# Kernel optimization log

Hardware: AMD Instinct MI355X
Metric: run time of the kernel (lower is better)

Reference implementation:

```python
import jax, jax.numpy as jnp
import numpy as np

L, M, K, H, F, D = 8, 32768, 8, 128, 32, 3  # fronts, nodes/front, in-degree, hidden, feat, depth-branches


def _resnet(x, w1, b1, w2, b2, w3, b3):
    # resnet module: lay3(tanh(lay2(tanh(lay1(x)))) + x)
    h1 = jnp.tanh(x @ w1 + b1)
    h2 = jnp.tanh(h1 @ w2 + b2)
    return (h2 + x) @ w3 + b3


def setup_inputs() -> dict:
    key = jax.random.key(0)
    ks = iter(jax.random.split(key, 80))

    def nrm(shape, fan_in):
        return jax.random.normal(next(ks), shape, jnp.float32) / np.float32(np.sqrt(fan_in))

    def bias(shape):
        return 0.01 * jax.random.normal(next(ks), shape, jnp.float32)

    inp = {}
    inp["node_feats"] = jax.random.normal(next(ks), (L, M, F), jnp.float32)
    inp["pred_idx"] = jax.random.randint(next(ks), (L - 1, M, K), 0, M, jnp.int32)
    inp["embed_w"] = nrm((F, H), F); inp["embed_b"] = bias((H,))
    # d{1,2,3}_mp_bwd and d{1,2,3}_mp_bwd1 : per-depth pair of H-resnets, stacked [D,2,...]
    inp["mp_w1"] = nrm((D, 2, H, H), H); inp["mp_b1"] = bias((D, 2, H))
    inp["mp_w2"] = nrm((D, 2, H, H), H); inp["mp_b2"] = bias((D, 2, H))
    inp["mp_w3"] = nrm((D, 2, H, H), H); inp["mp_b3"] = bias((D, 2, H))
    for p in ("comb", "node"):  # d*_comb_embed(+1), d*_node_embeds(+1)
        inp[p + "_wide_w1"] = nrm((D, 2 * H, 2 * H), 2 * H); inp[p + "_wide_b1"] = bias((D, 2 * H))
        inp[p + "_wide_w2"] = nrm((D, 2 * H, 2 * H), 2 * H); inp[p + "_wide_b2"] = bias((D, 2 * H))
        inp[p + "_wide_w3"] = nrm((D, 2 * H, H), 2 * H);     inp[p + "_wide_b3"] = bias((D, H))
        inp[p + "_h_w1"] = nrm((D, H, H), H); inp[p + "_h_b1"] = bias((D, H))
        inp[p + "_h_w2"] = nrm((D, H, H), H); inp[p + "_h_b2"] = bias((D, H))
        inp[p + "_h_w3"] = nrm((D, H, H), H); inp[p + "_h_b3"] = bias((D, H))
    return inp


def reference(node_feats, pred_idx, embed_w, embed_b,
              mp_w1, mp_b1, mp_w2, mp_b2, mp_w3, mp_b3,
              comb_wide_w1, comb_wide_b1, comb_wide_w2, comb_wide_b2, comb_wide_w3, comb_wide_b3,
              comb_h_w1, comb_h_b1, comb_h_w2, comb_h_b2, comb_h_w3, comb_h_b3,
              node_wide_w1, node_wide_b1, node_wide_w2, node_wide_b2, node_wide_w3, node_wide_b3,
              node_h_w1, node_h_b1, node_h_w2, node_h_b2, node_h_w3, node_h_b3):
    # front 0 (topological roots): apply_func only -> tanh(embed_op(feats))
    e = jnp.tanh(node_feats[0] @ embed_w + embed_b)          # [M, H]
    outs = [e]
    prev = e
    for l in range(1, L):
        d = min(l - 1, 2)                                    # bwd_depth branch (d1/d2/d3)
        # msg_func + redux_func: gather mailbox from predecessor front, sum-reduce, MLP
        s = prev[pred_idx[l - 1]].sum(axis=1)                # [M, K, H] -> [M, H]
        r = jnp.tanh(_resnet(s, mp_w1[d, 0], mp_b1[d, 0], mp_w2[d, 0], mp_b2[d, 0], mp_w3[d, 0], mp_b3[d, 0]))
        r = jnp.tanh(_resnet(r, mp_w1[d, 1], mp_b1[d, 1], mp_w2[d, 1], mp_b2[d, 1], mp_w3[d, 1], mp_b3[d, 1]))
        # apply_func: embed, comb branch (bwd_node_embeds is all-zero for not-yet-processed nodes),
        # then node_embeds branch on cat(embeds, msgs_redux)
        e = jnp.tanh(node_feats[l] @ embed_w + embed_b)
        c = jnp.concatenate([e, jnp.zeros_like(e)], axis=-1)  # [M, 2H]
        e = jnp.tanh(_resnet(c, comb_wide_w1[d], comb_wide_b1[d], comb_wide_w2[d], comb_wide_b2[d], comb_wide_w3[d], comb_wide_b3[d]))
        e = jnp.tanh(_resnet(e, comb_h_w1[d], comb_h_b1[d], comb_h_w2[d], comb_h_b2[d], comb_h_w3[d], comb_h_b3[d]))
        c2 = jnp.concatenate([e, r], axis=-1)                 # [M, 2H]
        e = jnp.tanh(_resnet(c2, node_wide_w1[d], node_wide_b1[d], node_wide_w2[d], node_wide_b2[d], node_wide_w3[d], node_wide_b3[d]))
        e = jnp.tanh(_resnet(e, node_h_w1[d], node_h_b1[d], node_h_w2[d], node_h_b2[d], node_h_w3[d], node_h_b3[d]))
        outs.append(e)
        prev = e
    return jnp.stack(outs)                                    # graph.ndata['bwd_node_embeds'] : [L, M, H]
```

## Files before the change

kernel.cpp:

```cpp
#include <hip/hip_runtime.h>
#include <hip/hip_bf16.h>

#define M_NODES 32768

using f16x8 = __attribute__((ext_vector_type(8))) _Float16;
using f32x4 = __attribute__((ext_vector_type(4))) float;
typedef unsigned short u16;
typedef unsigned int   u32;

__device__ __forceinline__ u16 f2h(float f){
  _Float16 h = (_Float16)f;
  return __builtin_bit_cast(u16, h);
}
__device__ __forceinline__ float h2f(u16 h){
  return (float)__builtin_bit_cast(_Float16, h);
}
__device__ __forceinline__ float tanh_fast(float x){
  float t = __builtin_amdgcn_exp2f(x * 2.8853900817779268f);
  return 1.0f - 2.0f * __builtin_amdgcn_rcpf(t + 1.0f);
}

struct PrepPtrs { const float* p[16]; };

__global__ void prep_kernel(PrepPtrs pp, u16* ws){
  const int Bc[16] = {1,6,6,6,3,3,3,3,3,3,3,3,3,3,3,3};
  const int Kc[16] = {32,128,128,128,256,256,256,128,128,128,256,256,256,128,128,128};
  const int Nc[16] = {128,128,128,128,256,256,128,128,128,128,256,256,128,128,128,128};
  const int tot = 1576960;
  for (int i = blockIdx.x*blockDim.x + threadIdx.x; i < tot; i += gridDim.x*blockDim.x){
    int e = i, s = 0;
    while (true){ int sz = Bc[s]*Kc[s]*Nc[s]; if (e < sz) break; e -= sz; ++s; }
    int K = Kc[s], N = Nc[s];
    int kn = K*N;
    int b = e / kn; int r2 = e - b*kn;
    int n = r2 / K; int k = r2 - n*K;
    float v = pp.p[s][(size_t)b*kn + (size_t)k*N + n];
    ws[i] = f2h(v);
  }
}

__global__ __launch_bounds__(256) void front0_kernel(const float* __restrict__ feats,
                                                     const float* __restrict__ ew,
                                                     const float* __restrict__ eb,
                                                     float* __restrict__ out){
  __shared__ float fl[2048];
  const int brow = blockIdx.x * 64;
  const float* f0 = feats + (size_t)brow*32;
#pragma unroll
  for (int it = 0; it < 2; ++it){
    int idx = threadIdx.x + it*256;
    *(float4*)(&fl[idx*4]) = *(const float4*)(f0 + idx*4);
  }
  __syncthreads();
  const int col = threadIdx.x & 127, rh = threadIdx.x >> 7;
  float w[32];
#pragma unroll
  for (int k = 0; k < 32; ++k) w[k] = ew[k*128 + col];
  const float bv = eb[col];
  for (int r = 0; r < 32; ++r){
    int row = rh*32 + r;
    float acc = bv;
#pragma unroll
    for (int k = 0; k < 32; ++k) acc += fl[row*32 + k] * w[k];
    out[(size_t)(brow + row)*128 + col] = tanh_fast(acc);
  }
}

template<int KLOOP, int N, int WS, int AMODE, int RESMODE, int OUTMODE>
__device__ __forceinline__ void mm_stage(const u16* inA, u16* outB, const u16* resB,
                                         const u16* __restrict__ wt,
                                         const float* __restrict__ bias,
                                         float* gout, u16* WP)
{
  const int tid  = threadIdx.x;
  const int lane = tid & 63, wid = tid >> 6;
  const int mh = wid >> 2, nq = wid & 3;
  const int q = lane >> 4, c = lane & 15;
  constexpr int NT = N / 64;
  constexpr int NP = KLOOP / 32;
  const float* inAf = (const float*)inA;
  float*       outF = (float*)outB;
  const float* resF = (const float*)resB;

  f32x4 acc[4][NT];
#pragma unroll
  for (int m = 0; m < 4; ++m)
#pragma unroll
    for (int j = 0; j < NT; ++j) acc[m][j] = (f32x4){0.f,0.f,0.f,0.f};

  for (int kp = 0; kp < NP; ++kp){
#pragma unroll
    for (int it = 0; it < N/128; ++it){
      int tt = tid + it*512;
      int n = tt >> 2, ko = (tt & 3) * 8;
      uint4 v = *(const uint4*)(wt + (size_t)n*WS + kp*32 + ko);
      *(uint4*)(&WP[n*40 + ko]) = v;
    }
    __syncthreads();
    f16x8 bf[NT];
#pragma unroll
    for (int j = 0; j < NT; ++j){
      int nt = nq*2 + (j & 1) + (j >> 1) * 8;
      bf[j] = *(const f16x8*)(&WP[(nt*16 + c)*40 + q*8]);
    }
#pragma unroll
    for (int m = 0; m < 4; ++m){
      if (AMODE == 0){
        f16x8 af = *(const f16x8*)(&inA[(mh*64 + m*16 + c)*264 + kp*32 + q*8]);
#pragma unroll
        for (int j = 0; j < NT; ++j)
          acc[m][j] = __builtin_amdgcn_mfma_f32_16x16x32_f16(af, bf[j], acc[m][j], 0, 0, 0);
      } else {
        const float* ap = inAf + (mh*64 + m*16 + c)*132 + kp*32 + q*8;
        float4 x0 = *(const float4*)(ap);
        float4 x1 = *(const float4*)(ap + 4);
        float xs[8] = {x0.x,x0.y,x0.z,x0.w,x1.x,x1.y,x1.z,x1.w};
        f16x8 ah, al;
#pragma unroll
        for (int k = 0; k < 8; ++k){
          _Float16 hi = (_Float16)xs[k];
          ah[k] = hi;
          al[k] = (_Float16)(xs[k] - (float)hi);
        }
#pragma unroll
        for (int j = 0; j < NT; ++j){
          acc[m][j] = __builtin_amdgcn_mfma_f32_16x16x32_f16(ah, bf[j], acc[m][j], 0, 0, 0);
          acc[m][j] = __builtin_amdgcn_mfma_f32_16x16x32_f16(al, bf[j], acc[m][j], 0, 0, 0);
        }
      }
    }
    __syncthreads();
  }
#pragma unroll
  for (int j = 0; j < NT; ++j){
    int nt = nq*2 + (j & 1) + (j >> 1) * 8;
    int col = nt*16 + c;
    float bv = bias[col];
#pragma unroll
    for (int m = 0; m < 4; ++m){
#pragma unroll
      for (int r = 0; r < 4; ++r){
        int row = mh*64 + m*16 + q*4 + r;
        float v = tanh_fast(acc[m][j][r] + bv);
        if (RESMODE == 2)      v += h2f(resB[row*264 + col]);
        else if (RESMODE == 1){ if (col < 128) v += h2f(resB[row*264 + col]); }
        else if (RESMODE == 3) v += resF[row*132 + col];
        if (OUTMODE == 2)      gout[(size_t)row*128 + col] = v;
        else if (OUTMODE == 1) outF[row*132 + col] = v;
        else                   outB[row*264 + col] = f2h(v);
      }
    }
  }
}

__device__ __forceinline__ void embed_stage(const float* __restrict__ featsRow,
                                            u16* outB, const u16* __restrict__ wt,
                                            const float* __restrict__ bias, u16* WP)
{
  const int tid  = threadIdx.x;
  const int lane = tid & 63, wid = tid >> 6;
  const int mh = wid >> 2, nq = wid & 3;
  const int q = lane >> 4, c = lane & 15;
  {
    int n = tid >> 2, ko = (tid & 3) * 8;
    *(uint4*)(&WP[n*40 + ko]) = *(const uint4*)(wt + n*32 + ko);
  }
  __syncthreads();
  f16x8 bf[2];
#pragma unroll
  for (int j = 0; j < 2; ++j){
    int nt = nq*2 + j;
    bf[j] = *(const f16x8*)(&WP[(nt*16 + c)*40 + q*8]);
  }
  f32x4 acc[4][2];
#pragma unroll
  for (int m = 0; m < 4; ++m){ acc[m][0] = (f32x4){0,0,0,0}; acc[m][1] = (f32x4){0,0,0,0}; }
#pragma unroll
  for (int m = 0; m < 4; ++m){
    int row = mh*64 + m*16 + c;
    const float* fp = featsRow + (size_t)row*32 + q*8;
    float4 a0 = *(const float4*)(fp);
    float4 a1 = *(const float4*)(fp + 4);
    float xs[8] = {a0.x,a0.y,a0.z,a0.w,a1.x,a1.y,a1.z,a1.w};
    f16x8 ah, al;
#pragma unroll
    for (int k = 0; k < 8; ++k){
      _Float16 hi = (_Float16)xs[k];
      ah[k] = hi;
      al[k] = (_Float16)(xs[k] - (float)hi);
    }
#pragma unroll
    for (int j = 0; j < 2; ++j){
      acc[m][j] = __builtin_amdgcn_mfma_f32_16x16x32_f16(ah, bf[j], acc[m][j], 0, 0, 0);
      acc[m][j] = __builtin_amdgcn_mfma_f32_16x16x32_f16(al, bf[j], acc[m][j], 0, 0, 0);
    }
  }
  __syncthreads();
#pragma unroll
  for (int j = 0; j < 2; ++j){
    int nt = nq*2 + j;
    int col = nt*16 + c;
    float bv = bias[col];
#pragma unroll
    for (int m = 0; m < 4; ++m){
#pragma unroll
      for (int r = 0; r < 4; ++r){
        int row = mh*64 + m*16 + q*4 + r;
        outB[row*264 + col] = f2h(tanh_fast(acc[m][j][r] + bv));
      }
    }
  }
}

struct FrontArgs {
  const float* feats; const int* pred;
  const u16* ws;
  float* out;
  const float* embed_b;
  const float* mp_b1; const float* mp_b2; const float* mp_b3;
  const float* cw_b1; const float* cw_b2; const float* cw_b3;
  const float* ch_b1; const float* ch_b2; const float* ch_b3;
  const float* nw_b1; const float* nw_b2; const float* nw_b3;
  const float* nh_b1; const float* nh_b2; const float* nh_b3;
  int l, d;
};

__global__ __launch_bounds__(512, 1) void front_kernel(FrontArgs A)
{
  extern __shared__ u16 lds[];
  u16* P  = lds;
  u16* Q  = lds + 33792;
  u16* WP = lds + 67584;
  const int brow = blockIdx.x * 128;
  const int d = A.d;
  const u16* ws = A.ws;

  {
    float* Pf = (float*)P;
    const float* prev = A.out + (size_t)(A.l - 1) * M_NODES * 128;
    const int c4 = threadIdx.x & 31;
    const int r0 = threadIdx.x >> 5;
#pragma unroll
    for (int rr = 0; rr < 8; ++rr){
      int row = r0 + rr*16;
      const int* ip = A.pred + ((size_t)(A.l - 1) * M_NODES + brow + row) * 8;
      float sx=0.f, sy=0.f, sz=0.f, sw=0.f;
#pragma unroll
      for (int p = 0; p < 8; ++p){
        const float4 v = *(const float4*)(prev + (size_t)ip[p]*128 + c4*4);
        sx += v.x; sy += v.y; sz += v.z; sw += v.w;
      }
      float4 o = {sx, sy, sz, sw};
      *(float4*)(&Pf[row*132 + c4*4]) = o;
    }
  }
  __syncthreads();

  const int d0 = d*2, d1 = d*2 + 1;
  mm_stage<128,128,128, 1,0,0>(P, Q, nullptr, ws + 4096   + (size_t)d0*16384, A.mp_b1 + d0*128, nullptr, WP);
  mm_stage<128,128,128, 0,3,1>(Q, P, P,       ws + 102400 + (size_t)d0*16384, A.mp_b2 + d0*128, nullptr, WP);
  mm_stage<128,128,128, 1,0,0>(P, Q, nullptr, ws + 200704 + (size_t)d0*16384, A.mp_b3 + d0*128, nullptr, WP);
  mm_stage<128,128,128, 0,0,0>(Q, P, nullptr, ws + 4096   + (size_t)d1*16384, A.mp_b1 + d1*128, nullptr, WP);
  mm_stage<128,128,128, 0,2,1>(P, P, Q,       ws + 102400 + (size_t)d1*16384, A.mp_b2 + d1*128, nullptr, WP);
  mm_stage<128,128,128, 1,0,0>(P, Q + 128, nullptr, ws + 200704 + (size_t)d1*16384, A.mp_b3 + d1*128, nullptr, WP);

  embed_stage(A.feats + ((size_t)A.l * M_NODES + brow) * 32, Q, ws, A.embed_b, WP);

  mm_stage<128,256,256, 0,0,0>(Q, P, nullptr, ws + 299008 + (size_t)d*65536, A.cw_b1 + d*256, nullptr, WP);
  mm_stage<256,256,256, 0,1,0>(P, P, Q,       ws + 495616 + (size_t)d*65536, A.cw_b2 + d*256, nullptr, WP);
  mm_stage<256,128,256, 0,0,0>(P, Q, nullptr, ws + 692224 + (size_t)d*32768, A.cw_b3 + d*128, nullptr, WP);
  mm_stage<128,128,128, 0,0,0>(Q, P, nullptr, ws + 790528 + (size_t)d*16384, A.ch_b1 + d*128, nullptr, WP);
  mm_stage<128,128,128, 0,2,0>(P, P, Q,       ws + 839680 + (size_t)d*16384, A.ch_b2 + d*128, nullptr, WP);
  mm_stage<128,128,128, 0,0,0>(P, Q, nullptr, ws + 888832 + (size_t)d*16384, A.ch_b3 + d*128, nullptr, WP);
  mm_stage<256,256,256, 0,0,0>(Q, P, nullptr, ws + 937984  + (size_t)d*65536, A.nw_b1 + d*256, nullptr, WP);
  mm_stage<256,256,256, 0,2,0>(P, P, Q,       ws + 1134592 + (size_t)d*65536, A.nw_b2 + d*256, nullptr, WP);
  mm_stage<256,128,256, 0,0,0>(P, Q, nullptr, ws + 1331200 + (size_t)d*32768, A.nw_b3 + d*128, nullptr, WP);
  mm_stage<128,128,128, 0,0,0>(Q, P, nullptr, ws + 1429504 + (size_t)d*16384, A.nh_b1 + d*128, nullptr, WP);
  mm_stage<128,128,128, 0,2,0>(P, P, Q,       ws + 1478656 + (size_t)d*16384, A.nh_b2 + d*128, nullptr, WP);
  float* gout = A.out + ((size_t)A.l * M_NODES + brow) * 128;
  mm_stage<128,128,128, 0,0,2>(P, nullptr, nullptr, ws + 1527808 + (size_t)d*16384, A.nh_b3 + d*128, gout, WP);
}

extern "C" void kernel_launch(void* const* d_in, const int* in_sizes, int n_in,
                              void* d_out, int out_size, void* d_ws, size_t ws_size,
                              hipStream_t stream)
{
  (void)in_sizes; (void)n_in; (void)out_size; (void)ws_size;
  const float* feats = (const float*)d_in[0];
  const int*   pred  = (const int*)d_in[1];
  u16*   ws  = (u16*)d_ws;
  float* out = (float*)d_out;

  PrepPtrs pp;
  const int wIdx[16] = {2,4,6,8,10,12,14,16,18,20,22,24,26,28,30,32};
  for (int i = 0; i < 16; ++i) pp.p[i] = (const float*)d_in[wIdx[i]];
  prep_kernel<<<2048, 256, 0, stream>>>(pp, ws);

  front0_kernel<<<M_NODES/64, 256, 0, stream>>>(feats, (const float*)d_in[2], (const float*)d_in[3], out);

  const size_t LDSB = (size_t)(2*128*264 + 256*40) * sizeof(u16);
  (void)hipFuncSetAttribute((const void*)front_kernel,
                            hipFuncAttributeMaxDynamicSharedMemorySize, (int)LDSB);

  FrontArgs A;
  A.feats = feats; A.pred = pred; A.ws = ws; A.out = out;
  A.embed_b = (const float*)d_in[3];
  A.mp_b1 = (const float*)d_in[5];  A.mp_b2 = (const float*)d_in[7];  A.mp_b3 = (const float*)d_in[9];
  A.cw_b1 = (const float*)d_in[11]; A.cw_b2 = (const float*)d_in[13]; A.cw_b3 = (const float*)d_in[15];
  A.ch_b1 = (const float*)d_in[17]; A.ch_b2 = (const float*)d_in[19]; A.ch_b3 = (const float*)d_in[21];
  A.nw_b1 = (const float*)d_in[23]; A.nw_b2 = (const float*)d_in[25]; A.nw_b3 = (const float*)d_in[27];
  A.nh_b1 = (const float*)d_in[29]; A.nh_b2 = (const float*)d_in[31]; A.nh_b3 = (const float*)d_in[33];

  for (int l = 1; l < 8; ++l){
    A.l = l;
    A.d = (l - 1 < 2) ? (l - 1) : 2;
    front_kernel<<<M_NODES/128, 512, LDSB, stream>>>(A);
  }
}
```

Before: 772.0 us.

## Load weights directly into registers with prefetch; shrink blocks to 64 rows

Weight tiles are no longer staged through LDS. Each wave now loads its B fragments straight from global memory into registers, double-buffered two k-steps ahead, which removes the per-k-step __syncthreads pairs. Blocks shrink to 64 rows and 256 threads with a smaller LDS footprint, aiming for two blocks per CU. Barriers now sit only after each stage's epilogue and before in-place writes. The cost is more global/L2 traffic for weights, since they are no longer shared across the two row-halves, plus higher register pressure.

```diff
diff --git a/kernel.cpp b/kernel.cpp
--- a/kernel.cpp
+++ b/kernel.cpp
@@ -66,15 +66,14 @@
   }
 }
 
-template<int KLOOP, int N, int WS, int AMODE, int RESMODE, int OUTMODE>
+template<int KLOOP, int N, int WS, int AMODE, int RESMODE, int OUTMODE, bool INPLACE>
 __device__ __forceinline__ void mm_stage(const u16* inA, u16* outB, const u16* resB,
                                          const u16* __restrict__ wt,
                                          const float* __restrict__ bias,
-                                         float* gout, u16* WP)
+                                         float* gout)
 {
   const int tid  = threadIdx.x;
-  const int lane = tid & 63, wid = tid >> 6;
-  const int mh = wid >> 2, nq = wid & 3;
+  const int lane = tid & 63, nq = tid >> 6;
   const int q = lane >> 4, c = lane & 15;
   constexpr int NT = N / 64;
   constexpr int NP = KLOOP / 32;
@@ -82,36 +81,42 @@
   float*       outF = (float*)outB;
   const float* resF = (const float*)resB;
 
+  const u16* wrow[NT];
+#pragma unroll
+  for (int j = 0; j < NT; ++j){
+    int nt = nq*2 + (j & 1) + (j >> 1) * 8;
+    wrow[j] = wt + (size_t)(nt*16 + c)*WS + q*8;
+  }
+  f16x8 breg[2][NT];
+#pragma unroll
+  for (int j = 0; j < NT; ++j) breg[0][j] = *(const f16x8*)(wrow[j]);
+#pragma unroll
+  for (int j = 0; j < NT; ++j) breg[1][j] = *(const f16x8*)(wrow[j] + 32);
+
   f32x4 acc[4][NT];
 #pragma unroll
   for (int m = 0; m < 4; ++m)
 #pragma unroll
     for (int j = 0; j < NT; ++j) acc[m][j] = (f32x4){0.f,0.f,0.f,0.f};
 
+#pragma unroll
   for (int kp = 0; kp < NP; ++kp){
-#pragma unroll
-    for (int it = 0; it < N/128; ++it){
-      int tt = tid + it*512;
-      int n = tt >> 2, ko = (tt & 3) * 8;
-      uint4 v = *(const uint4*)(wt + (size_t)n*WS + kp*32 + ko);
-      *(uint4*)(&WP[n*40 + ko]) = v;
-    }
-    __syncthreads();
-    f16x8 bf[NT];
-#pragma unroll
-    for (int j = 0; j < NT; ++j){
-      int nt = nq*2 + (j & 1) + (j >> 1) * 8;
-      bf[j] = *(const f16x8*)(&WP[(nt*16 + c)*40 + q*8]);
+    f16x8 bc[NT];
+#pragma unroll
+    for (int j = 0; j < NT; ++j) bc[j] = breg[kp & 1][j];
+    if (kp + 2 < NP){
+#pragma unroll
+      for (int j = 0; j < NT; ++j) breg[kp & 1][j] = *(const f16x8*)(wrow[j] + (kp + 2)*32);
     }
 #pragma unroll
     for (int m = 0; m < 4; ++m){
       if (AMODE == 0){
-        f16x8 af = *(const f16x8*)(&inA[(mh*64 + m*16 + c)*264 + kp*32 + q*8]);
+        f16x8 af = *(const f16x8*)(&inA[(m*16 + c)*264 + kp*32 + q*8]);
 #pragma unroll
         for (int j = 0; j < NT; ++j)
-          acc[m][j] = __builtin_amdgcn_mfma_f32_16x16x32_f16(af, bf[j], acc[m][j], 0, 0, 0);
+          acc[m][j] = __builtin_amdgcn_mfma_f32_16x16x32_f16(af, bc[j], acc[m][j], 0, 0, 0);
       } else {
-        const float* ap = inAf + (mh*64 + m*16 + c)*132 + kp*32 + q*8;
+        const float* ap = inAf + (m*16 + c)*132 + kp*32 + q*8;
         float4 x0 = *(const float4*)(ap);
         float4 x1 = *(const float4*)(ap + 4);
         float xs[8] = {x0.x,x0.y,x0.z,x0.w,x1.x,x1.y,x1.z,x1.w};
@@ -124,13 +129,13 @@
         }
 #pragma unroll
         for (int j = 0; j < NT; ++j){
-          acc[m][j] = __builtin_amdgcn_mfma_f32_16x16x32_f16(ah, bf[j], acc[m][j], 0, 0, 0);
-          acc[m][j] = __builtin_amdgcn_mfma_f32_16x16x32_f16(al, bf[j], acc[m][j], 0, 0, 0);
+          acc[m][j] = __builtin_amdgcn_mfma_f32_16x16x32_f16(ah, bc[j], acc[m][j], 0, 0, 0);
+          acc[m][j] = __builtin_amdgcn_mfma_f32_16x16x32_f16(al, bc[j], acc[m][j], 0, 0, 0);
         }
       }
     }
-    __syncthreads();
-  }
+  }
+  if (INPLACE) __syncthreads();
 #pragma unroll
   for (int j = 0; j < NT; ++j){
     int nt = nq*2 + (j & 1) + (j >> 1) * 8;
@@ -140,7 +145,7 @@
     for (int m = 0; m < 4; ++m){
 #pragma unroll
       for (int r = 0; r < 4; ++r){
-        int row = mh*64 + m*16 + q*4 + r;
+        int row = m*16 + q*4 + r;
         float v = tanh_fast(acc[m][j][r] + bv);
         if (RESMODE == 2)      v += h2f(resB[row*264 + col]);
         else if (RESMODE == 1){ if (col < 128) v += h2f(resB[row*264 + col]); }
@@ -151,33 +156,28 @@
       }
     }
   }
+  __syncthreads();
 }
 
 __device__ __forceinline__ void embed_stage(const float* __restrict__ featsRow,
                                             u16* outB, const u16* __restrict__ wt,
-                                            const float* __restrict__ bias, u16* WP)
+                                            const float* __restrict__ bias)
 {
   const int tid  = threadIdx.x;
-  const int lane = tid & 63, wid = tid >> 6;
-  const int mh = wid >> 2, nq = wid & 3;
+  const int lane = tid & 63, nq = tid >> 6;
   const int q = lane >> 4, c = lane & 15;
-  {
-    int n = tid >> 2, ko = (tid & 3) * 8;
-    *(uint4*)(&WP[n*40 + ko]) = *(const uint4*)(wt + n*32 + ko);
-  }
-  __syncthreads();
   f16x8 bf[2];
 #pragma unroll
   for (int j = 0; j < 2; ++j){
     int nt = nq*2 + j;
-    bf[j] = *(const f16x8*)(&WP[(nt*16 + c)*40 + q*8]);
+    bf[j] = *(const f16x8*)(wt + (nt*16 + c)*32 + q*8);
   }
   f32x4 acc[4][2];
 #pragma unroll
   for (int m = 0; m < 4; ++m){ acc[m][0] = (f32x4){0,0,0,0}; acc[m][1] = (f32x4){0,0,0,0}; }
 #pragma unroll
   for (int m = 0; m < 4; ++m){
-    int row = mh*64 + m*16 + c;
+    int row = m*16 + c;
     const float* fp = featsRow + (size_t)row*32 + q*8;
     float4 a0 = *(const float4*)(fp);
     float4 a1 = *(const float4*)(fp + 4);
@@ -195,7 +195,6 @@
       acc[m][j] = __builtin_amdgcn_mfma_f32_16x16x32_f16(al, bf[j], acc[m][j], 0, 0, 0);
     }
   }
-  __syncthreads();
 #pragma unroll
   for (int j = 0; j < 2; ++j){
     int nt = nq*2 + j;
@@ -205,11 +204,12 @@
     for (int m = 0; m < 4; ++m){
 #pragma unroll
       for (int r = 0; r < 4; ++r){
-        int row = mh*64 + m*16 + q*4 + r;
+        int row = m*16 + q*4 + r;
         outB[row*264 + col] = f2h(tanh_fast(acc[m][j][r] + bv));
       }
     }
   }
+  __syncthreads();
 }
 
 struct FrontArgs {
@@ -225,13 +225,12 @@
   int l, d;
 };
 
-__global__ __launch_bounds__(512, 1) void front_kernel(FrontArgs A)
+__global__ __launch_bounds__(256, 2) void front_kernel(FrontArgs A)
 {
   extern __shared__ u16 lds[];
   u16* P  = lds;
-  u16* Q  = lds + 33792;
-  u16* WP = lds + 67584;
-  const int brow = blockIdx.x * 128;
+  u16* Q  = lds + 16896;
+  const int brow = blockIdx.x * 64;
   const int d = A.d;
   const u16* ws = A.ws;
 
@@ -242,7 +241,7 @@
     const int r0 = threadIdx.x >> 5;
 #pragma unroll
     for (int rr = 0; rr < 8; ++rr){
-      int row = r0 + rr*16;
+      int row = r0 + rr*8;
       const int* ip = A.pred + ((size_t)(A.l - 1) * M_NODES + brow + row) * 8;
       float sx=0.f, sy=0.f, sz=0.f, sw=0.f;
 #pragma unroll
@@ -257,28 +256,26 @@
   __syncthreads();
 
   const int d0 = d*2, d1 = d*2 + 1;
-  mm_stage<128,128,128, 1,0,0>(P, Q, nullptr, ws + 4096   + (size_t)d0*16384, A.mp_b1 + d0*128, nullptr, WP);
-  mm_stage<128,128,128, 0,3,1>(Q, P, P,       ws + 102400 + (size_t)d0*16384, A.mp_b2 + d0*128, nullptr, WP);
-  mm_stage<128,128,128, 1,0,0>(P, Q, nullptr, ws + 200704 + (size_t)d0*16384, A.mp_b3 + d0*128, nullptr, WP);
-  mm_stage<128,128,128, 0,0,0>(Q, P, nullptr, ws + 4096   + (size_t)d1*16384, A.mp_b1 + d1*128, nullptr, WP);
-  mm_stage<128,128,128, 0,2,1>(P, P, Q,       ws + 102400 + (size_t)d1*16384, A.mp_b2 + d1*128, nullptr, WP);
-  mm_stage<128,128,128, 1,0,0>(P, Q + 128, nullptr, ws + 200704 + (size_t)d1*16384, A.mp_b3 + d1*128, nullptr, WP);
-
-  embed_stage(A.feats + ((size_t)A.l * M_NODES + brow) * 32, Q, ws, A.embed_b, WP);
-
-  mm_stage<128,256,256, 0,0,0>(Q, P, nullptr, ws + 299008 + (size_t)d*65536, A.cw_b1 + d*256, nullptr, WP);
-  mm_stage<256,256,256, 0,1,0>(P, P, Q,       ws + 495616 + (size_t)d*65536, A.cw_b2 + d*256, nullptr, WP);
-  mm_stage<256,128,256, 0,0,0>(P, Q, nullptr, ws + 692224 + (size_t)d*32768, A.cw_b3 + d*128, nullptr, WP);
-  mm_stage<128,128,128, 0,0,0>(Q, P, nullptr, ws + 790528 + (size_t)d*16384, A.ch_b1 + d*128, nullptr, WP);
-  mm_stage<128,128,128, 0,2,0>(P, P, Q,       ws + 839680 + (size_t)d*16384, A.ch_b2 + d*128, nullptr, WP);
-  mm_stage<128,128,128, 0,0,0>(P, Q, nullptr, ws + 888832 + (size_t)d*16384, A.ch_b3 + d*128, nullptr, WP);
-  mm_stage<256,256,256, 0,0,0>(Q, P, nullptr, ws + 937984  + (size_t)d*65536, A.nw_b1 + d*256, nullptr, WP);
-  mm_stage<256,256,256, 0,2,0>(P, P, Q,       ws + 1134592 + (size_t)d*65536, A.nw_b2 + d*256, nullptr, WP);
-  mm_stage<256,128,256, 0,0,0>(P, Q, nullptr, ws + 1331200 + (size_t)d*32768, A.nw_b3 + d*128, nullptr, WP);
-  mm_stage<128,128,128, 0,0,0>(Q, P, nullptr, ws + 1429504 + (size_t)d*16384, A.nh_b1 + d*128, nullptr, WP);
-  mm_stage<128,128,128, 0,2,0>(P, P, Q,       ws + 1478656 + (size_t)d*16384, A.nh_b2 + d*128, nullptr, WP);
+  mm_stage<128,128,128, 1,0,0,false>(P, Q, nullptr, ws + 4096   + (size_t)d0*16384, A.mp_b1 + d0*128, nullptr);
+  mm_stage<128,128,128, 0,3,1,false>(Q, P, P,       ws + 102400 + (size_t)d0*16384, A.mp_b2 + d0*128, nullptr);
+  mm_stage<128,128,128, 1,0,0,false>(P, Q, nullptr, ws + 200704 + (size_t)d0*16384, A.mp_b3 + d0*128, nullptr);
+  mm_stage<128,128,128, 0,0,0,false>(Q, P, nullptr, ws + 4096   + (size_t)d1*16384, A.mp_b1 + d1*128, nullptr);
+  mm_stage<128,128,128, 0,2,1,true >(P, P, Q,       ws + 102400 + (size_t)d1*16384, A.mp_b2 + d1*128, nullptr);
+  mm_stage<128,128,128, 1,0,0,false>(P, Q + 128, nullptr, ws + 200704 + (size_t)d1*16384, A.mp_b3 + d1*128, nullptr);
+  embed_stage(A.feats + ((size_t)A.l * M_NODES + brow) * 32, Q, ws, A.embed_b);
+  mm_stage<128,256,256, 0,0,0,false>(Q, P, nullptr, ws + 299008 + (size_t)d*65536, A.cw_b1 + d*256, nullptr);
+  mm_stage<256,256,256, 0,1,0,true >(P, P, Q,       ws + 495616 + (size_t)d*65536, A.cw_b2 + d*256, nullptr);
+  mm_stage<256,128,256, 0,0,0,false>(P, Q, nullptr, ws + 692224 + (size_t)d*32768, A.cw_b3 + d*128, nullptr);
+  mm_stage<128,128,128, 0,0,0,false>(Q, P, nullptr, ws + 790528 + (size_t)d*16384, A.ch_b1 + d*128, nullptr);
+  mm_stage<128,128,128, 0,2,0,true >(P, P, Q,       ws + 839680 + (size_t)d*16384, A.ch_b2 + d*128, nullptr);
+  mm_stage<128,128,128, 0,0,0,false>(P, Q, nullptr, ws + 888832 + (size_t)d*16384, A.ch_b3 + d*128, nullptr);
+  mm_stage<256,256,256, 0,0,0,false>(Q, P, nullptr, ws + 937984  + (size_t)d*65536, A.nw_b1 + d*256, nullptr);
+  mm_stage<256,256,256, 0,2,0,true >(P, P, Q,       ws + 1134592 + (size_t)d*65536, A.nw_b2 + d*256, nullptr);
+  mm_stage<256,128,256, 0,0,0,false>(P, Q, nullptr, ws + 1331200 + (size_t)d*32768, A.nw_b3 + d*128, nullptr);
+  mm_stage<128,128,128, 0,0,0,false>(Q, P, nullptr, ws + 1429504 + (size_t)d*16384, A.nh_b1 + d*128, nullptr);
+  mm_stage<128,128,128, 0,2,0,true >(P, P, Q,       ws + 1478656 + (size_t)d*16384, A.nh_b2 + d*128, nullptr);
   float* gout = A.out + ((size_t)A.l * M_NODES + brow) * 128;
-  mm_stage<128,128,128, 0,0,2>(P, nullptr, nullptr, ws + 1527808 + (size_t)d*16384, A.nh_b3 + d*128, gout, WP);
+  mm_stage<128,128,128, 0,0,2,false>(P, nullptr, nullptr, ws + 1527808 + (size_t)d*16384, A.nh_b3 + d*128, gout);
 }
 
 extern "C" void kernel_launch(void* const* d_in, const int* in_sizes, int n_in,
@@ -298,7 +295,7 @@
 
   front0_kernel<<<M_NODES/64, 256, 0, stream>>>(feats, (const float*)d_in[2], (const float*)d_in[3], out);
 
-  const size_t LDSB = (size_t)(2*128*264 + 256*40) * sizeof(u16);
+  const size_t LDSB = (size_t)(2*64*264) * sizeof(u16);
   (void)hipFuncSetAttribute((const void*)front_kernel,
                             hipFuncAttributeMaxDynamicSharedMemorySize, (int)LDSB);
 
@@ -314,6 +311,6 @@
   for (int l = 1; l < 8; ++l){
     A.l = l;
     A.d = (l - 1 < 2) ? (l - 1) : 2;
-    front_kernel<<<M_NODES/128, 512, LDSB, stream>>>(A);
-  }
-}
+    front_kernel<<<M_NODES/64, 256, LDSB, stream>>>(A);
+  }
+}
```

After: 700.6 us. -9.2%, faster.
